# Optimization experiments

Hardware: AMD Instinct MI355X
Metric: run time of the kernel (lower is better)

The kernel has to match this reference:

```python
import jax, jax.numpy as jnp
import numpy as np

LN_EPS = 1e-5
RMS_EPS = 1.1920929e-07  # torch.finfo(float32).eps (RMSNorm default eps=None)


def _layernorm(x, g, b):
    m = jnp.mean(x, axis=-1, keepdims=True)
    xc = x - m
    v = jnp.mean(xc * xc, axis=-1, keepdims=True)
    return xc / jnp.sqrt(v + LN_EPS) * g + b


def setup_inputs() -> dict:
    key = jax.random.key(0)
    ks = jax.random.split(key, 8)
    L, D, H, M, B, S = 4, 512, 8, 2048, 4, 2048
    std = 0.02
    return {
        "x": jax.random.normal(ks[0], (B, S, D), dtype=jnp.float32),
        # torch nn.Linear weights are [out, in]
        "Wq": jax.random.normal(ks[1], (L, D, D), dtype=jnp.float32) * std,
        "Wk": jax.random.normal(ks[2], (L, D, D), dtype=jnp.float32) * std,
        "Wv": jax.random.normal(ks[3], (L, D, D), dtype=jnp.float32) * std,
        "rms_w": jnp.ones((L, H, D // H), dtype=jnp.float32),
        "Wo": jax.random.normal(ks[4], (L, D, D), dtype=jnp.float32) * std,
        "bo": jnp.zeros((L, D), dtype=jnp.float32),
        "diffw": jnp.full((L,), 0.2, dtype=jnp.float32),
        "g_ffn": jnp.ones((L, D), dtype=jnp.float32),
        "b_ffn": jnp.zeros((L, D), dtype=jnp.float32),
        "W1": jax.random.normal(ks[5], (L, M, D), dtype=jnp.float32) * std,
        "b1": jnp.zeros((L, M), dtype=jnp.float32),
        "W2": jax.random.normal(ks[6], (L, D, M), dtype=jnp.float32) * std,
        "b2": jnp.zeros((L, D), dtype=jnp.float32),
        "g_f": jnp.ones((D,), dtype=jnp.float32),
        "b_f": jnp.zeros((D,), dtype=jnp.float32),
    }


def reference(x, Wq, Wk, Wv, rms_w, Wo, bo, diffw, g_ffn, b_ffn, W1, b1, W2, b2, g_f, b_f):
    def layer(xc, p):
        wq, wk, wv, rw, wo, bob, dw, g1, bn1, w1, bb1, w2, bb2 = p
        B, S, D = xc.shape
        H = rw.shape[0]
        F = D // (2 * H)  # per-component head dim (q/k split in two)
        qs = (xc @ wq.T).reshape(B, S, H, 2, F)
        ks_ = (xc @ wk.T).reshape(B, S, H, 2, F)
        scores = jnp.einsum('bqhif,bkhif->ibhqk', qs, ks_) * (F ** -0.5)
        atts = jax.nn.softmax(scores, axis=-1)  # [2,B,H,S,S]
        att = atts[0] - dw * atts[1]  # differential attention
        vs = (xc @ wv.T).reshape(B, S, H, D // H)
        o = jnp.einsum('bhqk,bkhe->bqhe', att, vs)  # [B,S,H,D/H]
        # fused per-token RMSNorm over (heads, head_dim)
        o = o / jnp.sqrt(jnp.mean(o * o, axis=(-2, -1), keepdims=True) + RMS_EPS) * rw
        xa = (o.reshape(B, S, D) @ wo.T + bob) * (1.0 - dw)
        xc = xa + xc  # attn residual
        h = _layernorm(xc, g1, bn1)
        h = jax.nn.gelu(h @ w1.T + bb1, approximate=False)
        xc = (h @ w2.T + bb2) + xc  # ffn residual
        return xc, None

    xf, _ = jax.lax.scan(layer, x, (Wq, Wk, Wv, rms_w, Wo, bo, diffw, g_ffn, b_ffn, W1, b1, W2, b2))
    return _layernorm(xf, g_f, b_f)
```

## Files before the change

kernel.cpp:

```cpp
#include <hip/hip_runtime.h>
#include <math.h>

#define B_ 4
#define S_ 2048
#define D_ 512
#define H_ 8
#define E_ 64
#define M_ 2048
#define L_ 4
#define R_ (B_ * S_)
#define RD_ ((size_t)R_ * D_)

typedef unsigned short u16;
typedef short short8 __attribute__((ext_vector_type(8)));
typedef float f32x4 __attribute__((ext_vector_type(4)));

__device__ __forceinline__ float4 ldg4(const float* p) {
    return *reinterpret_cast<const float4*>(p);
}
__device__ __forceinline__ float gelu_f(float x) {
    return 0.5f * x * (1.0f + erff(x * 0.70710678118654752440f));
}
__device__ __forceinline__ unsigned int cvt_pk_bf16(float lo, float hi) {
    unsigned int r;
    asm("v_cvt_pk_bf16_f32 %0, %1, %2" : "=v"(r) : "v"(lo), "v"(hi));
    return r;
}
__device__ __forceinline__ float fast_exp2(float x) {
    return __builtin_amdgcn_exp2f(x);
}
__device__ __forceinline__ float bf2f(u16 u) {
    union { unsigned int i; float f; } v; v.i = ((unsigned int)u) << 16;
    return v.f;
}

#define LDT 40
template <int EPI, int TM>
__global__ __launch_bounds__(256) void gemm_bf16(
    const u16* __restrict__ A, const u16* __restrict__ W,
    const float* __restrict__ bias, const float* __restrict__ res,
    const float* __restrict__ dwp, float* __restrict__ Cf,
    u16* __restrict__ Cb, int M, int N, int K, int ldc)
{
    constexpr int BMv = TM * 32;
    __shared__ __align__(16) u16 As[2][BMv * LDT];
    __shared__ __align__(16) u16 Bs[2][128 * LDT];

    const int t  = threadIdx.x;
    const int w  = t >> 6, l = t & 63;
    const int lr = l & 15, lk8 = (l >> 4) << 3;
    const int wr = (w >> 1) * (TM * 16), wc = (w & 1) * 64;
    const int bm = blockIdx.x * BMv, bn = blockIdx.y * 128;

    int arow, acol;
    if constexpr (TM == 4) { arow = t >> 1; acol = (t & 1) << 4; }
    else                   { arow = t >> 2; acol = (t & 3) << 3; }
    const int brow = t >> 1, bcol = (t & 1) << 4;

    const u16* Ag = A + (size_t)(bm + arow) * K + acol;
    const u16* Wg = W + (size_t)(bn + brow) * K + bcol;

    f32x4 acc[TM][4];
#pragma unroll
    for (int m = 0; m < TM; ++m)
#pragma unroll
        for (int n = 0; n < 4; ++n) acc[m][n] = (f32x4){0.f, 0.f, 0.f, 0.f};

    constexpr int NA = (TM == 4) ? 2 : 1;
    short8 av[2], bv[2];
    av[0] = *reinterpret_cast<const short8*>(Ag);
    if (NA == 2) av[1] = *reinterpret_cast<const short8*>(Ag + 8);
    bv[0] = *reinterpret_cast<const short8*>(Wg);
    bv[1] = *reinterpret_cast<const short8*>(Wg + 8);

    const int sa = arow * LDT + acol;
    const int sb = brow * LDT + bcol;
    *reinterpret_cast<short8*>(&As[0][sa]) = av[0];
    if (NA == 2) *reinterpret_cast<short8*>(&As[0][sa + 8]) = av[1];
    *reinterpret_cast<short8*>(&Bs[0][sb]) = bv[0];
    *reinterpret_cast<short8*>(&Bs[0][sb + 8]) = bv[1];
    __syncthreads();

    const int NT = K >> 5;
    int cur = 0;
    for (int kt = 0; kt < NT; ++kt) {
        const bool pf = (kt + 1 < NT);
        if (pf) {
            const u16* An = Ag + ((kt + 1) << 5);
            const u16* Wn = Wg + ((kt + 1) << 5);
            av[0] = *reinterpret_cast<const short8*>(An);
            if (NA == 2) av[1] = *reinterpret_cast<const short8*>(An + 8);
            bv[0] = *reinterpret_cast<const short8*>(Wn);
            bv[1] = *reinterpret_cast<const short8*>(Wn + 8);
        }
        short8 af[TM], bfv[4];
#pragma unroll
        for (int m = 0; m < TM; ++m)
            af[m] = *reinterpret_cast<const short8*>(&As[cur][(wr + m * 16 + lr) * LDT + lk8]);
#pragma unroll
        for (int n = 0; n < 4; ++n)
            bfv[n] = *reinterpret_cast<const short8*>(&Bs[cur][(wc + n * 16 + lr) * LDT + lk8]);
#pragma unroll
        for (int m = 0; m < TM; ++m)
#pragma unroll
            for (int n = 0; n < 4; ++n)
                acc[m][n] = __builtin_amdgcn_mfma_f32_16x16x32_bf16(af[m], bfv[n], acc[m][n], 0, 0, 0);
        if (pf) {
            *reinterpret_cast<short8*>(&As[cur ^ 1][sa]) = av[0];
            if (NA == 2) *reinterpret_cast<short8*>(&As[cur ^ 1][sa + 8]) = av[1];
            *reinterpret_cast<short8*>(&Bs[cur ^ 1][sb]) = bv[0];
            *reinterpret_cast<short8*>(&Bs[cur ^ 1][sb + 8]) = bv[1];
        }
        __syncthreads();
        cur ^= 1;
    }

    float sc1 = 1.f;
    if constexpr (EPI == 1) sc1 = 1.f - dwp[0];
    float bcolv[4] = {0.f, 0.f, 0.f, 0.f};
    if constexpr (EPI >= 1) {
#pragma unroll
        for (int n = 0; n < 4; ++n) bcolv[n] = bias[bn + wc + n * 16 + lr];
    }
#pragma unroll
    for (int m = 0; m < TM; ++m) {
        const int row0 = bm + wr + m * 16 + (l >> 4) * 4;
#pragma unroll
        for (int n = 0; n < 4; ++n) {
            const int col = bn + wc + n * 16 + lr;
            float vv[4];
#pragma unroll
            for (int q = 0; q < 4; ++q) {
                const int row = row0 + q;
                float v = acc[m][n][q];
                if constexpr (EPI >= 1) v += bcolv[n];
                if constexpr (EPI == 1) v = v * sc1 + res[(size_t)row * N + col];
                if constexpr (EPI == 2) v = gelu_f(v);
                if constexpr (EPI == 3) v += res[(size_t)row * N + col];
                if constexpr (EPI == 1 || EPI == 3) Cf[(size_t)row * N + col] = v;
                vv[q] = v;
            }
            const unsigned int pa = cvt_pk_bf16(vv[0], vv[1]);
            const unsigned int pb = cvt_pk_bf16(vv[2], vv[3]);
            Cb[(size_t)(row0 + 0) * ldc + col] = (u16)pa;
            Cb[(size_t)(row0 + 1) * ldc + col] = (u16)(pa >> 16);
            Cb[(size_t)(row0 + 2) * ldc + col] = (u16)pb;
            Cb[(size_t)(row0 + 3) * ldc + col] = (u16)(pb >> 16);
        }
    }
}

#define LDSW 72
#define QKVLD 1536
__global__ __launch_bounds__(512) void attn_mfma(
    const u16* __restrict__ QKV, u16* __restrict__ O,
    const float* __restrict__ dwp)
{
    __shared__ __align__(16) u16 Ks[64][LDSW];
    __shared__ __align__(16) u16 Vt[64][LDSW];
    __shared__ __align__(16) u16 Ps[128][LDSW];

    const int t   = threadIdx.x;
    const int w   = t >> 6;
    const int l   = t & 63;
    const int lr  = l & 15;
    const int g   = l >> 4;
    const int lk8 = g << 3;

    const int d   = blockIdx.y * 16 + blockIdx.x;
    const int s   = d >> 3;
    const int bh  = (d & 7) * 4 + (s >> 4);
    const int qt  = s & 15;
    const int b   = bh >> 3, h = bh & 7;

    const float dw = dwp[0];
    const float C = 0.17677669529663687f * 1.44269504088896340736f;
    const size_t tokbase = (size_t)b * S_;

    const u16* qrow = QKV + (tokbase + (size_t)(qt * 128 + w * 16 + lr)) * QKVLD + h * E_;
    short8 qf[2];
    {
        short8 qr0 = *reinterpret_cast<const short8*>(qrow + lk8);
        short8 qr1 = *reinterpret_cast<const short8*>(qrow + 32 + lk8);
        uint4 u0, u1;
        u0.x = cvt_pk_bf16(bf2f((u16)qr0[0]) * C, bf2f((u16)qr0[1]) * C);
        u0.y = cvt_pk_bf16(bf2f((u16)qr0[2]) * C, bf2f((u16)qr0[3]) * C);
        u0.z = cvt_pk_bf16(bf2f((u16)qr0[4]) * C, bf2f((u16)qr0[5]) * C);
        u0.w = cvt_pk_bf16(bf2f((u16)qr0[6]) * C, bf2f((u16)qr0[7]) * C);
        u1.x = cvt_pk_bf16(bf2f((u16)qr1[0]) * C, bf2f((u16)qr1[1]) * C);
        u1.y = cvt_pk_bf16(bf2f((u16)qr1[2]) * C, bf2f((u16)qr1[3]) * C);
        u1.z = cvt_pk_bf16(bf2f((u16)qr1[4]) * C, bf2f((u16)qr1[5]) * C);
        u1.w = cvt_pk_bf16(bf2f((u16)qr1[6]) * C, bf2f((u16)qr1[7]) * C);
        qf[0] = *reinterpret_cast<short8*>(&u0);
        qf[1] = *reinterpret_cast<short8*>(&u1);
    }

    float lsum[2] = {0.f, 0.f};
    f32x4 oacc[2][4];
#pragma unroll
    for (int c = 0; c < 2; ++c)
#pragma unroll
        for (int et = 0; et < 4; ++et) oacc[c][et] = (f32x4){0.f, 0.f, 0.f, 0.f};

    const int sr   = t >> 3;
    const int sc0  = (t & 7) << 3;
    const int prow = w * 16 + lr;
    const int vbit = lr & 8;

    const u16* kbase = QKV + tokbase * QKVLD + h * E_ + 512 + sc0;

    {
        const u16* kp = kbase + (size_t)sr * QKVLD;
        short8 kv = *reinterpret_cast<const short8*>(kp);
        short8 vv = *reinterpret_cast<const short8*>(kp + 512);
        *reinterpret_cast<short8*>(&Ks[sr][sc0]) = kv;
        const int vcol = sr ^ sc0;
#pragma unroll
        for (int i = 0; i < 8; ++i)
            Vt[sc0 + i][vcol] = (u16)vv[i];
    }
    __syncthreads();

    const int NT = S_ / 64;
    short8 kv_n, vv_n;
    for (int kt = 0; kt < NT; ++kt) {
        const bool pf = (kt + 1 < NT);
        if (pf) {
            const u16* kp = kbase + (size_t)((kt + 1) * 64 + sr) * QKVLD;
            kv_n = *reinterpret_cast<const short8*>(kp);
            vv_n = *reinterpret_cast<const short8*>(kp + 512);
        }

        short8 vfr[4][2];
#pragma unroll
        for (int et = 0; et < 4; ++et) {
            const int vx = (et << 4) ^ vbit;
            vfr[et][0] = *reinterpret_cast<const short8*>(&Vt[et * 16 + lr][lk8 ^ vx]);
            vfr[et][1] = *reinterpret_cast<const short8*>(&Vt[et * 16 + lr][(32 + lk8) ^ vx]);
        }

#pragma unroll
        for (int c = 0; c < 2; ++c) {
            f32x4 sacc[4];
            const f32x4 zf = (f32x4){0.f, 0.f, 0.f, 0.f};
#pragma unroll
            for (int kc = 0; kc < 4; ++kc) {
                short8 kf = *reinterpret_cast<const short8*>(&Ks[kc * 16 + lr][c * 32 + lk8]);
                sacc[kc] = __builtin_amdgcn_mfma_f32_16x16x32_bf16(kf, qf[c], zf, 0, 0, 0);
            }
            float ls = 0.f;
#pragma unroll
            for (int kc = 0; kc < 4; ++kc) {
                float p0 = fast_exp2(sacc[kc][0]);
                float p1 = fast_exp2(sacc[kc][1]);
                float p2 = fast_exp2(sacc[kc][2]);
                float p3 = fast_exp2(sacc[kc][3]);
                ls += (p0 + p1) + (p2 + p3);
                uint2 pk;
                pk.x = cvt_pk_bf16(p0, p1);
                pk.y = cvt_pk_bf16(p2, p3);
                *reinterpret_cast<uint2*>(&Ps[prow][kc * 16 + (g << 2)]) = pk;
            }
            lsum[c] += ls;
            short8 pf0 = *reinterpret_cast<const short8*>(&Ps[prow][lk8]);
            short8 pf1 = *reinterpret_cast<const short8*>(&Ps[prow][32 + lk8]);
#pragma unroll
            for (int et = 0; et < 4; ++et) {
                oacc[c][et] = __builtin_amdgcn_mfma_f32_16x16x32_bf16(vfr[et][0], pf0, oacc[c][et], 0, 0, 0);
                oacc[c][et] = __builtin_amdgcn_mfma_f32_16x16x32_bf16(vfr[et][1], pf1, oacc[c][et], 0, 0, 0);
            }
        }

        if (pf) {
            __syncthreads();
            *reinterpret_cast<short8*>(&Ks[sr][sc0]) = kv_n;
            const int vcol = sr ^ sc0;
#pragma unroll
            for (int i = 0; i < 8; ++i)
                Vt[sc0 + i][vcol] = (u16)vv_n[i];
            __syncthreads();
        }
    }

#pragma unroll
    for (int c = 0; c < 2; ++c) {
        lsum[c] += __shfl_xor(lsum[c], 16, 64);
        lsum[c] += __shfl_xor(lsum[c], 32, 64);
    }
    const float inv0 = 1.f / lsum[0];
    const float inv1 = dw / lsum[1];

    const size_t row = tokbase + (size_t)(qt * 128 + w * 16 + lr);
    u16* op = O + row * D_ + h * E_ + (g << 2);
#pragma unroll
    for (int et = 0; et < 4; ++et) {
        uint2 ov;
        ov.x = cvt_pk_bf16(oacc[0][et][0] * inv0 - oacc[1][et][0] * inv1,
                           oacc[0][et][1] * inv0 - oacc[1][et][1] * inv1);
        ov.y = cvt_pk_bf16(oacc[0][et][2] * inv0 - oacc[1][et][2] * inv1,
                           oacc[0][et][3] * inv0 - oacc[1][et][3] * inv1);
        *reinterpret_cast<uint2*>(op + et * 16) = ov;
    }
}

__global__ __launch_bounds__(256) void rmsnorm_bf(
    u16* __restrict__ X, const float* __restrict__ rw)
{
    const int row  = (blockIdx.x << 2) + (threadIdx.x >> 6);
    const int lane = threadIdx.x & 63;
    u16* xp = X + (size_t)row * D_ + lane * 8;
    short8 xv = *reinterpret_cast<const short8*>(xp);
    float xf[8];
#pragma unroll
    for (int i = 0; i < 8; ++i) xf[i] = bf2f((u16)xv[i]);
    float q = 0.f;
#pragma unroll
    for (int i = 0; i < 8; ++i) q += xf[i] * xf[i];
#pragma unroll
    for (int o = 1; o < 64; o <<= 1) q += __shfl_xor(q, o, 64);
    const float rstd = rsqrtf(q * (1.0f / 512.0f) + 1.1920929e-07f);
    const float* wp = rw + lane * 8;
    float4 w0 = ldg4(wp), w1 = ldg4(wp + 4);
    uint4 yv;
    yv.x = cvt_pk_bf16(xf[0] * rstd * w0.x, xf[1] * rstd * w0.y);
    yv.y = cvt_pk_bf16(xf[2] * rstd * w0.z, xf[3] * rstd * w0.w);
    yv.z = cvt_pk_bf16(xf[4] * rstd * w1.x, xf[5] * rstd * w1.y);
    yv.w = cvt_pk_bf16(xf[6] * rstd * w1.z, xf[7] * rstd * w1.w);
    *reinterpret_cast<uint4*>(xp) = yv;
}

template <int OUT>
__global__ __launch_bounds__(256) void layernorm_k(
    const float* __restrict__ X, const float* __restrict__ g,
    const float* __restrict__ bb, float* __restrict__ Yf,
    u16* __restrict__ Yb, float eps)
{
    const int row  = (blockIdx.x << 2) + (threadIdx.x >> 6);
    const int lane = threadIdx.x & 63;
    const float* xp = X + (size_t)row * D_;
    float4 x0 = ldg4(xp + lane * 4);
    float4 x1 = ldg4(xp + 256 + lane * 4);

    float s = x0.x + x0.y + x0.z + x0.w + x1.x + x1.y + x1.z + x1.w;
#pragma unroll
    for (int o = 1; o < 64; o <<= 1) s += __shfl_xor(s, o, 64);
    const float mean = s * (1.0f / 512.0f);

    x0.x -= mean; x0.y -= mean; x0.z -= mean; x0.w -= mean;
    x1.x -= mean; x1.y -= mean; x1.z -= mean; x1.w -= mean;
    float q = x0.x * x0.x + x0.y * x0.y + x0.z * x0.z + x0.w * x0.w
            + x1.x * x1.x + x1.y * x1.y + x1.z * x1.z + x1.w * x1.w;
#pragma unroll
    for (int o = 1; o < 64; o <<= 1) q += __shfl_xor(q, o, 64);
    const float rstd = rsqrtf(q * (1.0f / 512.0f) + eps);

    float4 g0 = ldg4(g + lane * 4),  g1 = ldg4(g + 256 + lane * 4);
    float4 b0 = ldg4(bb + lane * 4), b1 = ldg4(bb + 256 + lane * 4);
    float y[8];
    y[0] = x0.x * rstd * g0.x + b0.x; y[1] = x0.y * rstd * g0.y + b0.y;
    y[2] = x0.z * rstd * g0.z + b0.z; y[3] = x0.w * rstd * g0.w + b0.w;
    y[4] = x1.x * rstd * g1.x + b1.x; y[5] = x1.y * rstd * g1.y + b1.y;
    y[6] = x1.z * rstd * g1.z + b1.z; y[7] = x1.w * rstd * g1.w + b1.w;
    if constexpr (OUT == 0) {
        float* yp = Yf + (size_t)row * D_;
        *reinterpret_cast<float4*>(yp + lane * 4)       = make_float4(y[0], y[1], y[2], y[3]);
        *reinterpret_cast<float4*>(yp + 256 + lane * 4) = make_float4(y[4], y[5], y[6], y[7]);
    } else {
        u16* yp = Yb + (size_t)row * D_;
        uint2 a, b;
        a.x = cvt_pk_bf16(y[0], y[1]); a.y = cvt_pk_bf16(y[2], y[3]);
        b.x = cvt_pk_bf16(y[4], y[5]); b.y = cvt_pk_bf16(y[6], y[7]);
        *reinterpret_cast<uint2*>(yp + lane * 4)       = a;
        *reinterpret_cast<uint2*>(yp + 256 + lane * 4) = b;
    }
}

__global__ __launch_bounds__(256) void initcvt(
    const float* __restrict__ x, float* __restrict__ xc, u16* __restrict__ xcb)
{
    const size_t i = ((size_t)blockIdx.x * 256 + threadIdx.x) * 4;
    float4 v = ldg4(x + i);
    *reinterpret_cast<float4*>(xc + i) = v;
    uint2 o;
    o.x = cvt_pk_bf16(v.x, v.y); o.y = cvt_pk_bf16(v.z, v.w);
    *reinterpret_cast<uint2*>(xcb + i) = o;
}

__global__ __launch_bounds__(256) void conv_layer_w(
    const float* __restrict__ Wq, const float* __restrict__ Wk,
    const float* __restrict__ Wv, const float* __restrict__ Wo,
    const float* __restrict__ W1, const float* __restrict__ W2,
    u16* __restrict__ wqkv, u16* __restrict__ wo,
    u16* __restrict__ w1, u16* __restrict__ w2)
{
    const size_t i = ((size_t)blockIdx.x * 256 + threadIdx.x) * 4;
    const float* src; u16* dst;
    if (i < 786432) {
        dst = wqkv + i;
        if (i < 262144)      src = Wq + i;
        else if (i < 524288) src = Wk + (i - 262144);
        else                 src = Wv + (i - 524288);
    } else if (i < 1048576) { src = Wo + (i - 786432);  dst = wo + (i - 786432); }
    else if (i < 2097152)   { src = W1 + (i - 1048576); dst = w1 + (i - 1048576); }
    else                    { src = W2 + (i - 2097152); dst = w2 + (i - 2097152); }
    float4 v = ldg4(src);
    uint2 o;
    o.x = cvt_pk_bf16(v.x, v.y); o.y = cvt_pk_bf16(v.z, v.w);
    *reinterpret_cast<uint2*>(dst) = o;
}

extern "C" void kernel_launch(void* const* d_in, const int* in_sizes, int n_in,
                              void* d_out, int out_size, void* d_ws, size_t ws_size,
                              hipStream_t stream)
{
    const float* x     = (const float*)d_in[0];
    const float* Wq    = (const float*)d_in[1];
    const float* Wk    = (const float*)d_in[2];
    const float* Wv    = (const float*)d_in[3];
    const float* rms_w = (const float*)d_in[4];
    const float* Wo    = (const float*)d_in[5];
    const float* bo    = (const float*)d_in[6];
    const float* diffw = (const float*)d_in[7];
    const float* g_ffn = (const float*)d_in[8];
    const float* b_ffn = (const float*)d_in[9];
    const float* W1    = (const float*)d_in[10];
    const float* b1    = (const float*)d_in[11];
    const float* W2    = (const float*)d_in[12];
    const float* b2    = (const float*)d_in[13];
    const float* g_f   = (const float*)d_in[14];
    const float* b_f   = (const float*)d_in[15];

    char* ws = (char*)d_ws;
    float* xc   = (float*)(ws);
    u16*   xcb  = (u16*)(ws + 16777216);
    u16*   qkvb = (u16*)(ws + 25165824);
    u16*   ob   = (u16*)(ws + 50331648);
    u16*   tb   = qkvb;
    u16*   hb   = (u16*)(ws + 33554432);
    u16*   wqkv = (u16*)(ws + 67108864);
    u16*   wo_b = (u16*)(ws + 68681728);
    u16*   w1_b = (u16*)(ws + 69206016);
    u16*   w2_b = (u16*)(ws + 71303168);

    const dim3 blk(256);
    initcvt<<<dim3(RD_ / 4 / 256), blk, 0, stream>>>(x, xc, xcb);

    const dim3 g_tok(R_ / 4);

    for (int l = 0; l < L_; ++l) {
        const float* bo_l = bo + (size_t)l * D_;
        const float* b1_l = b1 + (size_t)l * M_;
        const float* b2_l = b2 + (size_t)l * D_;
        const float* dw_l = diffw + l;

        conv_layer_w<<<dim3(3072), blk, 0, stream>>>(
            Wq + (size_t)l * D_ * D_, Wk + (size_t)l * D_ * D_,
            Wv + (size_t)l * D_ * D_, Wo + (size_t)l * D_ * D_,
            W1 + (size_t)l * M_ * D_, W2 + (size_t)l * D_ * M_,
            wqkv, wo_b, w1_b, w2_b);

        gemm_bf16<0, 4><<<dim3(R_ / 128, 12), blk, 0, stream>>>(
            xcb, wqkv, nullptr, nullptr, nullptr, nullptr, qkvb,
            R_, 1536, D_, 1536);

        attn_mfma<<<dim3(S_ / 128, B_ * H_), dim3(512), 0, stream>>>(qkvb, ob, dw_l);

        rmsnorm_bf<<<g_tok, blk, 0, stream>>>(ob, rms_w + (size_t)l * D_);

        gemm_bf16<1, 2><<<dim3(R_ / 64, 4), blk, 0, stream>>>(
            ob, wo_b, bo_l, xc, dw_l, xc, xcb, R_, D_, D_, D_);

        layernorm_k<1><<<g_tok, blk, 0, stream>>>(
            xc, g_ffn + (size_t)l * D_, b_ffn + (size_t)l * D_, nullptr, tb, 1e-5f);

        gemm_bf16<2, 4><<<dim3(R_ / 128, 16), blk, 0, stream>>>(
            tb, w1_b, b1_l, nullptr, nullptr, nullptr, hb, R_, M_, D_, M_);

        gemm_bf16<3, 2><<<dim3(R_ / 64, 4), blk, 0, stream>>>(
            hb, w2_b, b2_l, xc, nullptr, xc, xcb, R_, D_, M_, D_);
    }

    layernorm_k<0><<<g_tok, blk, 0, stream>>>(xc, g_f, b_f, (float*)d_out, nullptr, 1e-5f);
}
```

Before: 802.6 us.

## Stage GEMM tiles via direct global-to-LDS async loads and retile output GEMMs

The bf16 GEMM now uses global_load_lds 16-byte copies to move A and W tiles straight into shared memory. This replaces the old path of loading into registers and then storing to LDS. The padded LDS layout (stride 40) becomes an unpadded 32-wide layout, so that each wave-uniform LDS base plus lane offset maps onto the tile. The tile shape is now parameterized by N-width: 128x128 for the QKV and FFN1 GEMMs, and 128x64 for the Wo and FFN2 GEMMs, which were 64x128 before. The intent is to free registers and VALU/LDS-store instructions, but the unpadded layout may add LDS bank conflicts on the fragment reads.

```diff
diff --git a/kernel.cpp b/kernel.cpp
--- a/kernel.cpp
+++ b/kernel.cpp
@@ -33,100 +33,95 @@
     union { unsigned int i; float f; } v; v.i = ((unsigned int)u) << 16;
     return v.f;
 }
-
-#define LDT 40
-template <int EPI, int TM>
+__device__ __forceinline__ void async_copy16(const u16* g, u16* l) {
+    auto* gp = reinterpret_cast<const __attribute__((address_space(1))) unsigned int*>(
+        reinterpret_cast<uintptr_t>(g));
+    auto* lp = reinterpret_cast<__attribute__((address_space(3))) unsigned int*>(
+        reinterpret_cast<uintptr_t>(l));
+    __builtin_amdgcn_global_load_lds(gp, lp, 16, 0, 0);
+}
+
+template <int EPI, int NB>
 __global__ __launch_bounds__(256) void gemm_bf16(
     const u16* __restrict__ A, const u16* __restrict__ W,
     const float* __restrict__ bias, const float* __restrict__ res,
     const float* __restrict__ dwp, float* __restrict__ Cf,
     u16* __restrict__ Cb, int M, int N, int K, int ldc)
 {
-    constexpr int BMv = TM * 32;
-    __shared__ __align__(16) u16 As[2][BMv * LDT];
-    __shared__ __align__(16) u16 Bs[2][128 * LDT];
+    constexpr int TN = NB / 32;
+    __shared__ __align__(16) u16 As[2][128 * 32];
+    __shared__ __align__(16) u16 Bs[2][NB * 32];
 
     const int t  = threadIdx.x;
     const int w  = t >> 6, l = t & 63;
-    const int lr = l & 15, lk8 = (l >> 4) << 3;
-    const int wr = (w >> 1) * (TM * 16), wc = (w & 1) * 64;
-    const int bm = blockIdx.x * BMv, bn = blockIdx.y * 128;
-
-    int arow, acol;
-    if constexpr (TM == 4) { arow = t >> 1; acol = (t & 1) << 4; }
-    else                   { arow = t >> 2; acol = (t & 3) << 3; }
-    const int brow = t >> 1, bcol = (t & 1) << 4;
-
-    const u16* Ag = A + (size_t)(bm + arow) * K + acol;
-    const u16* Wg = W + (size_t)(bn + brow) * K + bcol;
-
-    f32x4 acc[TM][4];
-#pragma unroll
-    for (int m = 0; m < TM; ++m)
-#pragma unroll
-        for (int n = 0; n < 4; ++n) acc[m][n] = (f32x4){0.f, 0.f, 0.f, 0.f};
-
-    constexpr int NA = (TM == 4) ? 2 : 1;
-    short8 av[2], bv[2];
-    av[0] = *reinterpret_cast<const short8*>(Ag);
-    if (NA == 2) av[1] = *reinterpret_cast<const short8*>(Ag + 8);
-    bv[0] = *reinterpret_cast<const short8*>(Wg);
-    bv[1] = *reinterpret_cast<const short8*>(Wg + 8);
-
-    const int sa = arow * LDT + acol;
-    const int sb = brow * LDT + bcol;
-    *reinterpret_cast<short8*>(&As[0][sa]) = av[0];
-    if (NA == 2) *reinterpret_cast<short8*>(&As[0][sa + 8]) = av[1];
-    *reinterpret_cast<short8*>(&Bs[0][sb]) = bv[0];
-    *reinterpret_cast<short8*>(&Bs[0][sb + 8]) = bv[1];
+    const int lr = l & 15, g = l >> 4;
+    const int wr = (w >> 1) * 64, wc = (w & 1) * (NB / 2);
+    const int bm = blockIdx.x * 128, bn = blockIdx.y * NB;
+
+    const u16* gA0 = A + (size_t)(bm + (t >> 2)) * K + (t & 3) * 8;
+    const u16* gA1 = A + (size_t)(bm + 64 + (t >> 2)) * K + (t & 3) * 8;
+    const u16* gB0 = W + (size_t)(bn + (t >> 2)) * K + (t & 3) * 8;
+    const u16* gB1 = gB0;
+    if constexpr (NB == 128) gB1 = W + (size_t)(bn + 64 + (t >> 2)) * K + (t & 3) * 8;
+
+    f32x4 acc[4][TN];
+#pragma unroll
+    for (int m = 0; m < 4; ++m)
+#pragma unroll
+        for (int n = 0; n < TN; ++n) acc[m][n] = (f32x4){0.f, 0.f, 0.f, 0.f};
+
+    {
+        u16* ab = &As[0][0];
+        async_copy16(gA0, ab + w * 512);
+        async_copy16(gA1, ab + 2048 + w * 512);
+        u16* bb = &Bs[0][0];
+        async_copy16(gB0, bb + w * 512);
+        if constexpr (NB == 128) async_copy16(gB1, bb + 2048 + w * 512);
+    }
     __syncthreads();
 
     const int NT = K >> 5;
     int cur = 0;
     for (int kt = 0; kt < NT; ++kt) {
-        const bool pf = (kt + 1 < NT);
-        if (pf) {
-            const u16* An = Ag + ((kt + 1) << 5);
-            const u16* Wn = Wg + ((kt + 1) << 5);
-            av[0] = *reinterpret_cast<const short8*>(An);
-            if (NA == 2) av[1] = *reinterpret_cast<const short8*>(An + 8);
-            bv[0] = *reinterpret_cast<const short8*>(Wn);
-            bv[1] = *reinterpret_cast<const short8*>(Wn + 8);
-        }
-        short8 af[TM], bfv[4];
-#pragma unroll
-        for (int m = 0; m < TM; ++m)
-            af[m] = *reinterpret_cast<const short8*>(&As[cur][(wr + m * 16 + lr) * LDT + lk8]);
-#pragma unroll
-        for (int n = 0; n < 4; ++n)
-            bfv[n] = *reinterpret_cast<const short8*>(&Bs[cur][(wc + n * 16 + lr) * LDT + lk8]);
-#pragma unroll
-        for (int m = 0; m < TM; ++m)
-#pragma unroll
-            for (int n = 0; n < 4; ++n)
+        if (kt + 1 < NT) {
+            const int off = (kt + 1) << 5;
+            u16* ab = &As[cur ^ 1][0];
+            async_copy16(gA0 + off, ab + w * 512);
+            async_copy16(gA1 + off, ab + 2048 + w * 512);
+            u16* bb = &Bs[cur ^ 1][0];
+            async_copy16(gB0 + off, bb + w * 512);
+            if constexpr (NB == 128) async_copy16(gB1 + off, bb + 2048 + w * 512);
+        }
+        short8 af[4], bfv[TN];
+#pragma unroll
+        for (int m = 0; m < 4; ++m)
+            af[m] = *reinterpret_cast<const short8*>(&As[cur][(wr + m * 16 + lr) * 32 + g * 8]);
+#pragma unroll
+        for (int n = 0; n < TN; ++n)
+            bfv[n] = *reinterpret_cast<const short8*>(&Bs[cur][(wc + n * 16 + lr) * 32 + g * 8]);
+#pragma unroll
+        for (int m = 0; m < 4; ++m)
+#pragma unroll
+            for (int n = 0; n < TN; ++n)
                 acc[m][n] = __builtin_amdgcn_mfma_f32_16x16x32_bf16(af[m], bfv[n], acc[m][n], 0, 0, 0);
-        if (pf) {
-            *reinterpret_cast<short8*>(&As[cur ^ 1][sa]) = av[0];
-            if (NA == 2) *reinterpret_cast<short8*>(&As[cur ^ 1][sa + 8]) = av[1];
-            *reinterpret_cast<short8*>(&Bs[cur ^ 1][sb]) = bv[0];
-            *reinterpret_cast<short8*>(&Bs[cur ^ 1][sb + 8]) = bv[1];
-        }
         __syncthreads();
         cur ^= 1;
     }
 
     float sc1 = 1.f;
     if constexpr (EPI == 1) sc1 = 1.f - dwp[0];
-    float bcolv[4] = {0.f, 0.f, 0.f, 0.f};
+    float bcolv[TN];
+#pragma unroll
+    for (int n = 0; n < TN; ++n) bcolv[n] = 0.f;
     if constexpr (EPI >= 1) {
 #pragma unroll
-        for (int n = 0; n < 4; ++n) bcolv[n] = bias[bn + wc + n * 16 + lr];
-    }
-#pragma unroll
-    for (int m = 0; m < TM; ++m) {
-        const int row0 = bm + wr + m * 16 + (l >> 4) * 4;
-#pragma unroll
-        for (int n = 0; n < 4; ++n) {
+        for (int n = 0; n < TN; ++n) bcolv[n] = bias[bn + wc + n * 16 + lr];
+    }
+#pragma unroll
+    for (int m = 0; m < 4; ++m) {
+        const int row0 = bm + wr + m * 16 + g * 4;
+#pragma unroll
+        for (int n = 0; n < TN; ++n) {
             const int col = bn + wc + n * 16 + lr;
             float vv[4];
 #pragma unroll
@@ -459,7 +454,7 @@
             W1 + (size_t)l * M_ * D_, W2 + (size_t)l * D_ * M_,
             wqkv, wo_b, w1_b, w2_b);
 
-        gemm_bf16<0, 4><<<dim3(R_ / 128, 12), blk, 0, stream>>>(
+        gemm_bf16<0, 128><<<dim3(R_ / 128, 12), blk, 0, stream>>>(
             xcb, wqkv, nullptr, nullptr, nullptr, nullptr, qkvb,
             R_, 1536, D_, 1536);
 
@@ -467,16 +462,16 @@
 
         rmsnorm_bf<<<g_tok, blk, 0, stream>>>(ob, rms_w + (size_t)l * D_);
 
-        gemm_bf16<1, 2><<<dim3(R_ / 64, 4), blk, 0, stream>>>(
+        gemm_bf16<1, 64><<<dim3(R_ / 128, 8), blk, 0, stream>>>(
             ob, wo_b, bo_l, xc, dw_l, xc, xcb, R_, D_, D_, D_);
 
         layernorm_k<1><<<g_tok, blk, 0, stream>>>(
             xc, g_ffn + (size_t)l * D_, b_ffn + (size_t)l * D_, nullptr, tb, 1e-5f);
 
-        gemm_bf16<2, 4><<<dim3(R_ / 128, 16), blk, 0, stream>>>(
+        gemm_bf16<2, 128><<<dim3(R_ / 128, 16), blk, 0, stream>>>(
             tb, w1_b, b1_l, nullptr, nullptr, nullptr, hb, R_, M_, D_, M_);
 
-        gemm_bf16<3, 2><<<dim3(R_ / 64, 4), blk, 0, stream>>>(
+        gemm_bf16<3, 64><<<dim3(R_ / 128, 8), blk, 0, stream>>>(
             hb, w2_b, b2_l, xc, nullptr, xc, xcb, R_, D_, M_, D_);
     }
 
```

New measurement: 788.1 us. About the same (-1.8%).
